# Kernel tuning notes

Measured on AMD Instinct MI355X. Metric: run time of the kernel, lower is better.

The kernel has to match this reference:

```python
import jax, jax.numpy as jnp
import numpy as np

N_NODES = 50000
N_EDGES = 600000
IN_FEATS = 16
H_FEAT = 128
N_CLASSES = 4
N_HIDDEN_LAYERS = 19  # conv2..conv20


def setup_inputs() -> dict:
    key = jax.random.key(0)
    ks = jax.random.split(key, 10)
    x = jax.random.normal(ks[0], (N_NODES, IN_FEATS), dtype=jnp.float32)
    edge_index = jax.random.randint(ks[1], (2, N_EDGES), 0, N_NODES, dtype=jnp.int32)
    edge_attr = jax.random.uniform(ks[2], (N_EDGES, 1), dtype=jnp.float32)
    s_in = 1.0 / np.sqrt(IN_FEATS)
    s_h = 1.0 / np.sqrt(H_FEAT)
    W_in = jax.random.uniform(ks[3], (IN_FEATS, H_FEAT), minval=-s_in, maxval=s_in, dtype=jnp.float32)
    b_in = jax.random.uniform(ks[4], (H_FEAT,), minval=-s_in, maxval=s_in, dtype=jnp.float32)
    W_h = jax.random.uniform(ks[5], (N_HIDDEN_LAYERS, H_FEAT, H_FEAT), minval=-s_h, maxval=s_h, dtype=jnp.float32)
    b_h = jax.random.uniform(ks[6], (N_HIDDEN_LAYERS, H_FEAT), minval=-s_h, maxval=s_h, dtype=jnp.float32)
    W_fc = jax.random.uniform(ks[7], (H_FEAT, N_CLASSES), minval=-s_h, maxval=s_h, dtype=jnp.float32)
    b_fc = jax.random.uniform(ks[8], (N_CLASSES,), minval=-s_h, maxval=s_h, dtype=jnp.float32)
    return {"x": x, "edge_index": edge_index, "edge_attr": edge_attr,
            "W_in": W_in, "b_in": b_in, "W_h": W_h, "b_h": b_h,
            "W_fc": W_fc, "b_fc": b_fc}


def reference(x, edge_index, edge_attr, W_in, b_in, W_h, b_h, W_fc, b_fc):
    src, dst = edge_index[0], edge_index[1]
    ew = edge_attr[:, 0]  # edge_weight = edge_attr[:, 0]
    n = x.shape[0]
    # degree by dst, clamped at 1
    deg = jax.ops.segment_sum(jnp.ones(src.shape[0], dtype=x.dtype), dst, num_segments=n)
    deg_inv = 1.0 / jnp.maximum(deg, 1.0)  # [N]

    def conv(h, W, b):
        h = h @ W + b                       # [N, out]
        msg = h[src] * ew[:, None]          # [E, out]
        agg = jax.ops.segment_sum(msg, dst, num_segments=n)
        return agg * deg_inv[:, None]

    h = jax.nn.leaky_relu(conv(x, W_in, b_in))

    def step(h, params):
        W, b = params
        return jax.nn.leaky_relu(conv(h, W, b)), None

    h, _ = jax.lax.scan(step, h, (W_h, b_h))
    return h @ W_fc + b_fc  # [N, num_classes]
```

## Files before the change

kernel.cpp:

```cpp
#include <hip/hip_runtime.h>
#include <hip/hip_fp16.h>

#define N_NODES 50000
#define N_EDGES 600000
#define IN_F 16
#define HF 128
#define NC 4
#define NHL 19
#define WS_STRIDE 136

__device__ __forceinline__ float lrelu(float x) { return x > 0.f ? x : 0.01f * x; }

struct h4 { __half2 a, b; };

typedef _Float16 f16;
typedef _Float16 f16x8 __attribute__((ext_vector_type(8)));
typedef float    f32x4 __attribute__((ext_vector_type(4)));


__global__ void count_deg_k(const int* __restrict__ dst, int* __restrict__ cnt) {
    int e = blockIdx.x * 256 + threadIdx.x;
    if (e < N_EDGES) atomicAdd(&cnt[dst[e]], 1);
}

__global__ void deginv_k(const int* __restrict__ cnt, float* __restrict__ dinv) {
    int v = blockIdx.x * 256 + threadIdx.x;
    if (v < N_NODES) dinv[v] = 1.0f / fmaxf((float)cnt[v], 1.0f);
}

__global__ void scan_k(const int* __restrict__ cnt, int* __restrict__ rowptr) {
    __shared__ int wsum[16];
    __shared__ int carry_s;
    int t = threadIdx.x;
    int lane = t & 63, wid = t >> 6;
    if (t == 0) carry_s = 0;
    __syncthreads();
    for (int base = 0; base < N_NODES; base += 4096) {
        int idx = base + t * 4;
        int4 v = make_int4(0, 0, 0, 0);
        if (idx + 3 < N_NODES) v = *(const int4*)&cnt[idx];
        else {
            if (idx     < N_NODES) v.x = cnt[idx];
            if (idx + 1 < N_NODES) v.y = cnt[idx + 1];
            if (idx + 2 < N_NODES) v.z = cnt[idx + 2];
            if (idx + 3 < N_NODES) v.w = cnt[idx + 3];
        }
        int s1 = v.x + v.y, s2 = s1 + v.z, total = s2 + v.w;
        int sc = total;
#pragma unroll
        for (int off = 1; off < 64; off <<= 1) {
            int u = __shfl_up(sc, off, 64);
            if (lane >= off) sc += u;
        }
        if (lane == 63) wsum[wid] = sc;
        __syncthreads();
        if (t < 16) {
            int w = wsum[t];
#pragma unroll
            for (int off = 1; off < 16; off <<= 1) {
                int u = __shfl_up(w, off, 64);
                if (t >= off) w += u;
            }
            wsum[t] = w;
        }
        __syncthreads();
        int prefix = carry_s + (wid > 0 ? wsum[wid - 1] : 0) + (sc - total);
        if (idx     < N_NODES) rowptr[idx]     = prefix;
        if (idx + 1 < N_NODES) rowptr[idx + 1] = prefix + v.x;
        if (idx + 2 < N_NODES) rowptr[idx + 2] = prefix + s1;
        if (idx + 3 < N_NODES) rowptr[idx + 3] = prefix + s2;
        __syncthreads();
        if (t == 0) carry_s += wsum[15];
        __syncthreads();
    }
    if (t == 0) rowptr[N_NODES] = carry_s;
}

__global__ void fill_k(const int* __restrict__ src, const int* __restrict__ dst,
                       const float* __restrict__ ea, const int* __restrict__ rowptr,
                       int* __restrict__ fill, int2* __restrict__ edg,
                       const float* __restrict__ dinv) {
    int e = blockIdx.x * 256 + threadIdx.x;
    if (e < N_EDGES) {
        int d = dst[e];
        int pos = rowptr[d] + atomicAdd(&fill[d], 1);
        edg[pos] = make_int2(src[e], __float_as_int(ea[e] * dinv[d]));
    }
}


__global__ void wconv_k(const float* __restrict__ Wh, __half* __restrict__ Wt) {
    int idx = blockIdx.x * 256 + threadIdx.x;
    if (idx >= NHL * HF * HF) return;
    int l = idx / (HF * HF);
    int r = idx - l * (HF * HF);
    int n = r >> 7;
    int k = r & 127;
    Wt[idx] = __float2half(Wh[(size_t)l * HF * HF + k * HF + n]);
}


__global__ void gemm_in_k(const float* __restrict__ X, const float* __restrict__ W,
                          const float* __restrict__ b, h4* __restrict__ Th) {
    __shared__ float Ws[IN_F * HF];
    int t = threadIdx.x;
    ((float4*)Ws)[t]       = ((const float4*)W)[t];
    ((float4*)Ws)[t + 256] = ((const float4*)W)[t + 256];
    __syncthreads();
    int row = blockIdx.x * 16 + (t >> 4);
    if (row >= N_NODES) return;
    int tx = t & 15;
    int c0 = tx * 4, c1 = 64 + tx * 4;
    float4 a0 = *(const float4*)&b[c0];
    float4 a1 = *(const float4*)&b[c1];
    const float4* xr = (const float4*)(X + row * IN_F);
#pragma unroll
    for (int k4 = 0; k4 < 4; k4++) {
        float4 xv = xr[k4];
        const float* xp = (const float*)&xv;
#pragma unroll
        for (int kk = 0; kk < 4; kk++) {
            int k = k4 * 4 + kk;
            float4 w0 = *(const float4*)&Ws[k * HF + c0];
            float4 w1 = *(const float4*)&Ws[k * HF + c1];
            float xs = xp[kk];
            a0.x = fmaf(xs, w0.x, a0.x); a0.y = fmaf(xs, w0.y, a0.y);
            a0.z = fmaf(xs, w0.z, a0.z); a0.w = fmaf(xs, w0.w, a0.w);
            a1.x = fmaf(xs, w1.x, a1.x); a1.y = fmaf(xs, w1.y, a1.y);
            a1.z = fmaf(xs, w1.z, a1.z); a1.w = fmaf(xs, w1.w, a1.w);
        }
    }
    h4 o0; o0.a = __floats2half2_rn(a0.x, a0.y); o0.b = __floats2half2_rn(a0.z, a0.w);
    h4 o1; o1.a = __floats2half2_rn(a1.x, a1.y); o1.b = __floats2half2_rn(a1.z, a1.w);
    Th[((size_t)row * HF + c0) >> 2] = o0;
    Th[((size_t)row * HF + c1) >> 2] = o1;
}


__global__ __launch_bounds__(256) void gemm_mfma_k(const __half* __restrict__ H,
                                                   const __half* __restrict__ Wt,
                                                   const float* __restrict__ b,
                                                   __half* __restrict__ T) {
    __shared__ __half Ws[HF * WS_STRIDE];
    __shared__ __half Hs[64 * WS_STRIDE];
    int t = threadIdx.x;
    int rbase = blockIdx.x * 64;
    int u16 = t & 15;
    int rg  = t >> 4;

#pragma unroll
    for (int p = 0; p < 8; p++) {
        int n = p * 16 + rg;
        *(float4*)&Ws[n * WS_STRIDE + u16 * 8] = *(const float4*)&Wt[(size_t)n * HF + u16 * 8];
    }
#pragma unroll
    for (int p = 0; p < 4; p++) {
        int rl = p * 16 + rg;
        int row = rbase + rl;
        if (row >= N_NODES) row = N_NODES - 1;
        *(float4*)&Hs[rl * WS_STRIDE + u16 * 8] = *(const float4*)&H[(size_t)row * HF + u16 * 8];
    }
    __syncthreads();

    int lane = t & 63;
    int w    = t >> 6;
    int wr   = w * 16;
    int m16  = lane & 15;
    int q    = lane >> 4;

    f16x8 af[4];
#pragma unroll
    for (int kc = 0; kc < 4; kc++)
        af[kc] = *(const f16x8*)&Hs[(wr + m16) * WS_STRIDE + kc * 32 + q * 8];

    f32x4 acc[8];
#pragma unroll
    for (int nt = 0; nt < 8; nt++) {
        float bv = b[nt * 16 + m16];
        acc[nt] = (f32x4){bv, bv, bv, bv};
#pragma unroll
        for (int kc = 0; kc < 4; kc++) {
            f16x8 bf = *(const f16x8*)&Ws[(nt * 16 + m16) * WS_STRIDE + kc * 32 + q * 8];
            acc[nt] = __builtin_amdgcn_mfma_f32_16x16x32_f16(af[kc], bf, acc[nt], 0, 0, 0);
        }
    }
    __syncthreads();

#pragma unroll
    for (int nt = 0; nt < 8; nt++)
#pragma unroll
        for (int r = 0; r < 4; r++)
            Hs[(wr + q * 4 + r) * WS_STRIDE + nt * 16 + m16] = __float2half(acc[nt][r]);
    __syncthreads();

#pragma unroll
    for (int p = 0; p < 4; p++) {
        int rl = p * 16 + rg;
        int row = rbase + rl;
        if (row < N_NODES)
            *(float4*)&T[(size_t)row * HF + u16 * 8] = *(float4*)&Hs[rl * WS_STRIDE + u16 * 8];
    }
}


__global__ __launch_bounds__(256) void agg2_k(const h4* __restrict__ Th, h4* __restrict__ O,
                                              const int* __restrict__ rowptr,
                                              const int2* __restrict__ edg) {
    int gw = blockIdx.x * 4 + (threadIdx.x >> 6);
    int vA = gw * 2;
    if (vA >= N_NODES) return;
    int lane = threadIdx.x & 63;
    int half = lane >> 5;
    int li   = lane & 31;

    int rA = __builtin_amdgcn_readfirstlane(rowptr[vA]);
    int rM = __builtin_amdgcn_readfirstlane(rowptr[vA + 1]);
    int rB = __builtin_amdgcn_readfirstlane(rowptr[vA + 2]);
    int eBase = half ? rM : rA;
    int eEnd  = half ? rB : rM;
    int degmax = max(rM - rA, rB - rM);
    int nb = (degmax + 15) >> 4;

    float4 acc = make_float4(0.f, 0.f, 0.f, 0.f);

    for (int eb = 0; eb < nb; eb++) {
        int idx = eBase + eb * 16 + (li & 15);
        bool ok = idx < eEnd;
        int2 rec = edg[ok ? idx : 0];
        int   s_l = rec.x;
        float w_l = ok ? __int_as_float(rec.y) : 0.f;
        int sb = half << 5;
#pragma unroll
        for (int g = 0; g < 2; g++) {
            int   ss[8];
            float ww[8];
#pragma unroll
            for (int u = 0; u < 8; u++) {
                int sl = sb + g * 8 + u;
                ss[u] = __shfl(s_l, sl, 64);
                ww[u] = __shfl(w_l, sl, 64);
            }
            h4 hv[8];
#pragma unroll
            for (int u = 0; u < 8; u++)
                hv[u] = Th[(size_t)ss[u] * (HF / 4) + li];
#pragma unroll
            for (int u = 0; u < 8; u++) {
                float2 p0 = __half22float2(hv[u].a);
                float2 p1 = __half22float2(hv[u].b);
                acc.x = fmaf(p0.x, ww[u], acc.x);
                acc.y = fmaf(p0.y, ww[u], acc.y);
                acc.z = fmaf(p1.x, ww[u], acc.z);
                acc.w = fmaf(p1.y, ww[u], acc.w);
            }
        }
    }
    int v = vA + half;
    h4 o;
    o.a = __floats2half2_rn(lrelu(acc.x), lrelu(acc.y));
    o.b = __floats2half2_rn(lrelu(acc.z), lrelu(acc.w));
    O[(size_t)v * (HF / 4) + li] = o;
}


__global__ void fc_k(const __half* __restrict__ H, const float* __restrict__ W,
                     const float* __restrict__ b, float* __restrict__ out) {
    int r = blockIdx.x * 256 + threadIdx.x;
    if (r >= N_NODES) return;
    float4 acc = *(const float4*)b;
    const h4* hp = (const h4*)(H + (size_t)r * HF);
    const float4* w4 = (const float4*)W;
#pragma unroll
    for (int k4 = 0; k4 < 32; k4++) {
        h4 hh = hp[k4];
        float2 p0 = __half22float2(hh.a);
        float2 p1 = __half22float2(hh.b);
        float4 wa = w4[k4 * 4 + 0], wb = w4[k4 * 4 + 1];
        float4 wc = w4[k4 * 4 + 2], wd = w4[k4 * 4 + 3];
        acc.x = fmaf(p0.x, wa.x, acc.x); acc.y = fmaf(p0.x, wa.y, acc.y);
        acc.z = fmaf(p0.x, wa.z, acc.z); acc.w = fmaf(p0.x, wa.w, acc.w);
        acc.x = fmaf(p0.y, wb.x, acc.x); acc.y = fmaf(p0.y, wb.y, acc.y);
        acc.z = fmaf(p0.y, wb.z, acc.z); acc.w = fmaf(p0.y, wb.w, acc.w);
        acc.x = fmaf(p1.x, wc.x, acc.x); acc.y = fmaf(p1.x, wc.y, acc.y);
        acc.z = fmaf(p1.x, wc.z, acc.z); acc.w = fmaf(p1.x, wc.w, acc.w);
        acc.x = fmaf(p1.y, wd.x, acc.x); acc.y = fmaf(p1.y, wd.y, acc.y);
        acc.z = fmaf(p1.y, wd.z, acc.z); acc.w = fmaf(p1.y, wd.w, acc.w);
    }
    *(float4*)&out[r * NC] = acc;
}


extern "C" void kernel_launch(void* const* d_in, const int* in_sizes, int n_in,
                              void* d_out, int out_size, void* d_ws, size_t ws_size,
                              hipStream_t stream) {
    const float* X   = (const float*)d_in[0];
    const int*   EI  = (const int*)d_in[1];
    const float* EA  = (const float*)d_in[2];
    const float* Win = (const float*)d_in[3];
    const float* bin = (const float*)d_in[4];
    const float* Wh  = (const float*)d_in[5];
    const float* bh  = (const float*)d_in[6];
    const float* Wfc = (const float*)d_in[7];
    const float* bfc = (const float*)d_in[8];
    float* out = (float*)d_out;
    const int* src = EI;
    const int* dst = EI + N_EDGES;

    char* ws = (char*)d_ws;
    size_t off = 0;
    __half* Oh  = (__half*)(ws + off); off += (size_t)N_NODES * HF * 2;
    __half* Th  = (__half*)(ws + off); off += (size_t)N_NODES * HF * 2;
    __half* Wt  = (__half*)(ws + off); off += (size_t)NHL * HF * HF * 2;
    int2* edg   = (int2*)(ws + off);  off += (size_t)N_EDGES * 8;
    int* rowptr = (int*)(ws + off);   off += (((size_t)(N_NODES + 1) * 4 + 15) / 16) * 16;
    int* cnt    = (int*)(ws + off);   off += (size_t)N_NODES * 4;
    int* fill   = (int*)(ws + off);   off += (size_t)N_NODES * 4;
    float* dinv = (float*)(ws + off); off += (size_t)N_NODES * 4;

    hipMemsetAsync(cnt, 0, N_NODES * 4, stream);
    hipMemsetAsync(fill, 0, N_NODES * 4, stream);
    count_deg_k<<<(N_EDGES + 255) / 256, 256, 0, stream>>>(dst, cnt);
    deginv_k<<<(N_NODES + 255) / 256, 256, 0, stream>>>(cnt, dinv);
    scan_k<<<1, 1024, 0, stream>>>(cnt, rowptr);
    fill_k<<<(N_EDGES + 255) / 256, 256, 0, stream>>>(src, dst, EA, rowptr, fill, edg, dinv);
    wconv_k<<<(NHL * HF * HF + 255) / 256, 256, 0, stream>>>(Wh, Wt);

    const int aggg  = (N_NODES / 2 + 3) / 4;
    const int gemmg = (N_NODES + 63) / 64;

    gemm_in_k<<<(N_NODES + 15) / 16, 256, 0, stream>>>(X, Win, bin, (h4*)Th);
    agg2_k<<<aggg, 256, 0, stream>>>((const h4*)Th, (h4*)Oh, rowptr, edg);
    for (int l = 0; l < NHL; l++) {
        gemm_mfma_k<<<gemmg, 256, 0, stream>>>(
            Oh, Wt + (size_t)l * HF * HF, bh + (size_t)l * HF, Th);
        agg2_k<<<aggg, 256, 0, stream>>>((const h4*)Th, (h4*)Oh, rowptr, edg);
    }
    fc_k<<<(N_NODES + 255) / 256, 256, 0, stream>>>(Oh, Wfc, bfc, out);
}
```

Measured before the change: 857.8 us.

## Fuse neighbor aggregation into the next layer's MFMA GEMM kernel

Each hidden layer now runs one kernel that gathers and aggregates neighbor features, applies leaky ReLU, stages the result in shared memory, and then multiplies it by the next weight matrix with MFMA. Two ping-pong buffers replace the intermediate aggregated tensor. Only one aggregation launch remains, before the final FC. This removes a full write and read of the aggregated feature matrix per layer plus a launch. In exchange, the latency-bound gather runs in far fewer, LDS-heavy blocks, which lowers the parallelism available to hide memory latency.

```diff
diff --git a/kernel.cpp b/kernel.cpp
--- a/kernel.cpp
+++ b/kernel.cpp
@@ -137,10 +137,12 @@
 }
 
 
-__global__ __launch_bounds__(256) void gemm_mfma_k(const __half* __restrict__ H,
-                                                   const __half* __restrict__ Wt,
-                                                   const float* __restrict__ b,
-                                                   __half* __restrict__ T) {
+__global__ __launch_bounds__(256) void fused_k(const __half* __restrict__ Tin,
+                                               const __half* __restrict__ Wt,
+                                               const float* __restrict__ b,
+                                               __half* __restrict__ Tout,
+                                               const int* __restrict__ rowptr,
+                                               const int2* __restrict__ edg) {
     __shared__ __half Ws[HF * WS_STRIDE];
     __shared__ __half Hs[64 * WS_STRIDE];
     int t = threadIdx.x;
@@ -153,20 +155,69 @@
         int n = p * 16 + rg;
         *(float4*)&Ws[n * WS_STRIDE + u16 * 8] = *(const float4*)&Wt[(size_t)n * HF + u16 * 8];
     }
-#pragma unroll
-    for (int p = 0; p < 4; p++) {
-        int rl = p * 16 + rg;
-        int row = rbase + rl;
-        if (row >= N_NODES) row = N_NODES - 1;
-        *(float4*)&Hs[rl * WS_STRIDE + u16 * 8] = *(const float4*)&H[(size_t)row * HF + u16 * 8];
-    }
-    __syncthreads();
 
     int lane = t & 63;
     int w    = t >> 6;
-    int wr   = w * 16;
-    int m16  = lane & 15;
-    int q    = lane >> 4;
+    int half = lane >> 5;
+    int li   = lane & 31;
+    const h4* Tin4 = (const h4*)Tin;
+
+#pragma unroll 1
+    for (int j = 0; j < 8; j++) {
+        int vA  = rbase + w * 16 + j * 2;
+        int vAc = min(vA, N_NODES - 2);
+        int rA = __builtin_amdgcn_readfirstlane(rowptr[vAc]);
+        int rM = __builtin_amdgcn_readfirstlane(rowptr[vAc + 1]);
+        int rB = __builtin_amdgcn_readfirstlane(rowptr[vAc + 2]);
+        int eBase = half ? rM : rA;
+        int eEnd  = half ? rB : rM;
+        int degmax = max(rM - rA, rB - rM);
+        int nb = (degmax + 15) >> 4;
+
+        float4 acc = make_float4(0.f, 0.f, 0.f, 0.f);
+        for (int eb = 0; eb < nb; eb++) {
+            int idx = eBase + eb * 16 + (li & 15);
+            bool ok = idx < eEnd;
+            int2 rec = edg[ok ? idx : 0];
+            int   s_l = rec.x;
+            float w_l = ok ? __int_as_float(rec.y) : 0.f;
+            int sb = half << 5;
+#pragma unroll
+            for (int g = 0; g < 2; g++) {
+                int   ss[8];
+                float ww[8];
+#pragma unroll
+                for (int u = 0; u < 8; u++) {
+                    int sl = sb + g * 8 + u;
+                    ss[u] = __shfl(s_l, sl, 64);
+                    ww[u] = __shfl(w_l, sl, 64);
+                }
+                h4 hv[8];
+#pragma unroll
+                for (int u = 0; u < 8; u++)
+                    hv[u] = Tin4[(size_t)ss[u] * (HF / 4) + li];
+#pragma unroll
+                for (int u = 0; u < 8; u++) {
+                    float2 p0 = __half22float2(hv[u].a);
+                    float2 p1 = __half22float2(hv[u].b);
+                    acc.x = fmaf(p0.x, ww[u], acc.x);
+                    acc.y = fmaf(p0.y, ww[u], acc.y);
+                    acc.z = fmaf(p1.x, ww[u], acc.z);
+                    acc.w = fmaf(p1.y, ww[u], acc.w);
+                }
+            }
+        }
+        h4 o;
+        o.a = __floats2half2_rn(lrelu(acc.x), lrelu(acc.y));
+        o.b = __floats2half2_rn(lrelu(acc.z), lrelu(acc.w));
+        int row = w * 16 + j * 2 + half;
+        *(h4*)&Hs[row * WS_STRIDE + li * 4] = o;
+    }
+    __syncthreads();
+
+    int wr  = w * 16;
+    int m16 = lane & 15;
+    int q   = lane >> 4;
 
     f16x8 af[4];
 #pragma unroll
@@ -198,7 +249,7 @@
         int rl = p * 16 + rg;
         int row = rbase + rl;
         if (row < N_NODES)
-            *(float4*)&T[(size_t)row * HF + u16 * 8] = *(float4*)&Hs[rl * WS_STRIDE + u16 * 8];
+            *(float4*)&Tout[(size_t)row * HF + u16 * 8] = *(float4*)&Hs[rl * WS_STRIDE + u16 * 8];
     }
 }
 
@@ -308,8 +359,9 @@
 
     char* ws = (char*)d_ws;
     size_t off = 0;
+    __half* Ta  = (__half*)(ws + off); off += (size_t)N_NODES * HF * 2;
+    __half* Tb  = (__half*)(ws + off); off += (size_t)N_NODES * HF * 2;
     __half* Oh  = (__half*)(ws + off); off += (size_t)N_NODES * HF * 2;
-    __half* Th  = (__half*)(ws + off); off += (size_t)N_NODES * HF * 2;
     __half* Wt  = (__half*)(ws + off); off += (size_t)NHL * HF * HF * 2;
     int2* edg   = (int2*)(ws + off);  off += (size_t)N_EDGES * 8;
     int* rowptr = (int*)(ws + off);   off += (((size_t)(N_NODES + 1) * 4 + 15) / 16) * 16;
@@ -326,14 +378,16 @@
     wconv_k<<<(NHL * HF * HF + 255) / 256, 256, 0, stream>>>(Wh, Wt);
 
     const int aggg  = (N_NODES / 2 + 3) / 4;
-    const int gemmg = (N_NODES + 63) / 64;
-
-    gemm_in_k<<<(N_NODES + 15) / 16, 256, 0, stream>>>(X, Win, bin, (h4*)Th);
-    agg2_k<<<aggg, 256, 0, stream>>>((const h4*)Th, (h4*)Oh, rowptr, edg);
+    const int fuseg = (N_NODES + 63) / 64;
+
+    gemm_in_k<<<(N_NODES + 15) / 16, 256, 0, stream>>>(X, Win, bin, (h4*)Ta);
+    __half* cur = Ta;
+    __half* nxt = Tb;
     for (int l = 0; l < NHL; l++) {
-        gemm_mfma_k<<<gemmg, 256, 0, stream>>>(
-            Oh, Wt + (size_t)l * HF * HF, bh + (size_t)l * HF, Th);
-        agg2_k<<<aggg, 256, 0, stream>>>((const h4*)Th, (h4*)Oh, rowptr, edg);
-    }
+        fused_k<<<fuseg, 256, 0, stream>>>(
+            cur, Wt + (size_t)l * HF * HF, bh + (size_t)l * HF, nxt, rowptr, edg);
+        __half* tmp = cur; cur = nxt; nxt = tmp;
+    }
+    agg2_k<<<aggg, 256, 0, stream>>>((const h4*)cur, (h4*)Oh, rowptr, edg);
     fc_k<<<(N_NODES + 255) / 256, 256, 0, stream>>>(Oh, Wfc, bfc, out);
 }
```

Result: slower. 912.9 us (+6.4%).
